# Performance work log

Hardware: AMD Instinct MI355X
Metric: run time of the kernel (lower is better)

Reference implementation:

```python
import jax, jax.numpy as jnp
import numpy as np

B, N, D, H = 8, 2048, 128, 128  # batch, num_nodes, input_size, hidden_size


def setup_inputs() -> dict:
    key = jax.random.key(0)
    ks = jax.random.split(key, 10)
    s = 1.0 / np.sqrt(H)
    u = lambda k, shape: jax.random.uniform(k, shape, jnp.float32, -s, s)
    return {
        "x": jax.random.normal(ks[0], (B, N, D), jnp.float32),
        "adj_matrix": jax.random.randint(ks[1], (B, N, N), 0, 2, jnp.int32),
        # PyTorch LSTM params, gate order (i, f, g, o); forward + backward dirs
        "w_ih_f": u(ks[2], (4 * H, D)),
        "w_hh_f": u(ks[3], (4 * H, H)),
        "b_ih_f": u(ks[4], (4 * H,)),
        "b_hh_f": u(ks[5], (4 * H,)),
        "w_ih_b": u(ks[6], (4 * H, D)),
        "w_hh_b": u(ks[7], (4 * H, H)),
        "b_ih_b": u(ks[8], (4 * H,)),
        "b_hh_b": u(ks[9], (4 * H,)),
    }


def _lstm_last_h(xp, w_hh):
    # xp: [T, B, 4H] precomputed input projection + biases; returns final h [B, H]
    b = xp.shape[1]
    h0 = jnp.zeros((b, H), xp.dtype)
    c0 = jnp.zeros((b, H), xp.dtype)

    def step(carry, xt):
        h, c = carry
        gates = xt + h @ w_hh.T
        i, f, g, o = jnp.split(gates, 4, axis=-1)
        c = jax.nn.sigmoid(f) * c + jax.nn.sigmoid(i) * jnp.tanh(g)
        h = jax.nn.sigmoid(o) * jnp.tanh(c)
        return (h, c), None

    (hT, _), _ = jax.lax.scan(step, (h0, c0), xp)
    return hT


def reference(x, adj_matrix, w_ih_f, w_hh_f, b_ih_f, b_hh_f, w_ih_b, w_hh_b, b_ih_b, b_hh_b):
    x = x.astype(jnp.float32)
    a = (adj_matrix > 0).astype(jnp.float32)  # [B, N, N]
    # mean over {self} + neighbors: (x_i + sum_j a_ij x_j) / (1 + deg_i)
    deg = a.sum(-1, keepdims=True)
    xa = (x + jnp.einsum('bij,bjd->bid', a, x)) / (1.0 + deg)  # [B, N, D]

    seq = jnp.swapaxes(xa, 0, 1)  # [N, B, D], time-major over nodes
    hT_f = _lstm_last_h(seq @ w_ih_f.T + (b_ih_f + b_hh_f), w_hh_f)
    hT_b = _lstm_last_h(seq[::-1] @ w_ih_b.T + (b_ih_b + b_hh_b), w_hh_b)
    return jnp.concatenate([hT_f, hT_b], axis=-1)  # [B, 2H]
```

## Files before the change

### kernel.cpp

```cpp
#include <hip/hip_runtime.h>
#include <math.h>

#define BB 8
#define NN 2048
#define DD 128
#define HH 128

typedef float f4 __attribute__((ext_vector_type(4)));

__device__ __forceinline__ float fast_rcp(float x) { return __builtin_amdgcn_rcpf(x); }

#define TI 32
#define TJ 64

__global__ __launch_bounds__(256) void k_agg(const float* __restrict__ x,
                                             const int* __restrict__ adj,
                                             float* __restrict__ xa) {
    __shared__ __align__(16) float xs[TJ][132];
    __shared__ __align__(16) float as[TI][68];
    const int b = blockIdx.y;
    const int i0 = blockIdx.x * TI;
    const int tid = threadIdx.x;
    const int ig = tid >> 5;
    const int dg = tid & 31;
    const float* xb = x + (size_t)b * NN * DD;
    const int* ab = adj + (size_t)b * NN * NN;

    float acc[4][4];
    float deg[4];
#pragma unroll
    for (int i = 0; i < 4; ++i) {
        deg[i] = 0.f;
#pragma unroll
        for (int d = 0; d < 4; ++d) acc[i][d] = 0.f;
    }

    for (int j0 = 0; j0 < NN; j0 += TJ) {
#pragma unroll
        for (int k = 0; k < 8; ++k) {
            int idx = tid + k * 256;
            int row = idx >> 5, c4 = idx & 31;
            float4 v = *(const float4*)(xb + (size_t)(j0 + row) * DD + c4 * 4);
            *(float4*)(&xs[row][c4 * 4]) = v;
        }
#pragma unroll
        for (int k = 0; k < 2; ++k) {
            int idx = tid + k * 256;
            int row = idx >> 4, c4 = idx & 15;
            int4 v = *(const int4*)(ab + (size_t)(i0 + row) * NN + j0 + c4 * 4);
            float4 f;
            f.x = v.x > 0 ? 1.f : 0.f;
            f.y = v.y > 0 ? 1.f : 0.f;
            f.z = v.z > 0 ? 1.f : 0.f;
            f.w = v.w > 0 ? 1.f : 0.f;
            *(float4*)(&as[row][c4 * 4]) = f;
        }
        __syncthreads();
#pragma unroll 4
        for (int jq = 0; jq < TJ; jq += 4) {
            float4 av[4], xv[4];
#pragma unroll
            for (int i = 0; i < 4; ++i) av[i] = *(const float4*)(&as[ig * 4 + i][jq]);
#pragma unroll
            for (int jj = 0; jj < 4; ++jj) xv[jj] = *(const float4*)(&xs[jq + jj][dg * 4]);
#pragma unroll
            for (int i = 0; i < 4; ++i) {
                const float* ap = (const float*)&av[i];
#pragma unroll
                for (int jj = 0; jj < 4; ++jj) {
                    float a = ap[jj];
                    const float* xp4 = (const float*)&xv[jj];
                    deg[i] += a;
                    acc[i][0] = fmaf(a, xp4[0], acc[i][0]);
                    acc[i][1] = fmaf(a, xp4[1], acc[i][1]);
                    acc[i][2] = fmaf(a, xp4[2], acc[i][2]);
                    acc[i][3] = fmaf(a, xp4[3], acc[i][3]);
                }
            }
        }
        __syncthreads();
    }
#pragma unroll
    for (int i = 0; i < 4; ++i) {
        int gi = i0 + ig * 4 + i;
        float r = fast_rcp(1.f + deg[i]);
        float4 xv = *(const float4*)(xb + (size_t)gi * DD + dg * 4);
        float4 o;
        o.x = (xv.x + acc[i][0]) * r;
        o.y = (xv.y + acc[i][1]) * r;
        o.z = (xv.z + acc[i][2]) * r;
        o.w = (xv.w + acc[i][3]) * r;
        *(float4*)(xa + ((size_t)b * NN + gi) * DD + dg * 4) = o;
    }
}

#define MT 64
#define GT 32

__global__ __launch_bounds__(256) void k_proj(const float* __restrict__ xa,
                                              const float* __restrict__ wif,
                                              const float* __restrict__ wib,
                                              const float* __restrict__ bif,
                                              const float* __restrict__ bhf,
                                              const float* __restrict__ bib,
                                              const float* __restrict__ bhb,
                                              float* __restrict__ xpf,
                                              float* __restrict__ xpb) {
    __shared__ __align__(16) float xs[MT][132];
    __shared__ __align__(16) float wl[GT][132];
    const int r0 = blockIdx.x * MT;
    const int g0 = blockIdx.y * GT;
    const int tid = threadIdx.x;
#pragma unroll
    for (int k = 0; k < 8; ++k) {
        int idx = tid + k * 256;
        int row = idx >> 5, c4 = idx & 31;
        int r = r0 + row;
        int t = r >> 3, bb = r & 7;
        float4 v = *(const float4*)(xa + ((size_t)bb * NN + t) * DD + c4 * 4);
        *(float4*)(&xs[row][c4 * 4]) = v;
    }
#pragma unroll
    for (int k = 0; k < 4; ++k) {
        int idx = tid + k * 256;
        int row = idx >> 5, c4 = idx & 31;
        int g = g0 + row;
        const float* wsrc = (g < 512) ? (wif + (size_t)g * DD) : (wib + (size_t)(g - 512) * DD);
        *(float4*)(&wl[row][c4 * 4]) = *(const float4*)(wsrc + c4 * 4);
    }
    __syncthreads();
    const int mg = tid >> 4;
    const int gg = tid & 15;
    float acc[4][2];
#pragma unroll
    for (int i = 0; i < 4; ++i) { acc[i][0] = 0.f; acc[i][1] = 0.f; }
#pragma unroll 8
    for (int d4 = 0; d4 < 32; ++d4) {
        float4 xv[4], wv[2];
#pragma unroll
        for (int i = 0; i < 4; ++i) xv[i] = *(const float4*)(&xs[mg * 4 + i][d4 * 4]);
        wv[0] = *(const float4*)(&wl[gg * 2 + 0][d4 * 4]);
        wv[1] = *(const float4*)(&wl[gg * 2 + 1][d4 * 4]);
#pragma unroll
        for (int i = 0; i < 4; ++i) {
#pragma unroll
            for (int j = 0; j < 2; ++j) {
                acc[i][j] = fmaf(xv[i].x, wv[j].x, acc[i][j]);
                acc[i][j] = fmaf(xv[i].y, wv[j].y, acc[i][j]);
                acc[i][j] = fmaf(xv[i].z, wv[j].z, acc[i][j]);
                acc[i][j] = fmaf(xv[i].w, wv[j].w, acc[i][j]);
            }
        }
    }
#pragma unroll
    for (int j = 0; j < 2; ++j) {
        int g = g0 + gg * 2 + j;
        float bias = (g < 512) ? (bif[g] + bhf[g]) : (bib[g - 512] + bhb[g - 512]);
#pragma unroll
        for (int i = 0; i < 4; ++i) {
            int r = r0 + mg * 4 + i;
            int t = r >> 3, bb = r & 7;
            float v = acc[i][j] + bias;
            if (g < 512) {
                int p = 4 * (g & 127) + (g >> 7);
                xpf[((size_t)t * BB + bb) * 512 + p] = v;
            } else {
                int gb = g - 512;
                int p = 4 * (gb & 127) + (gb >> 7);
                xpb[((size_t)(NN - 1 - t) * BB + bb) * 512 + p] = v;
            }
        }
    }
}


#define STRG(x) #x
#define WLD(R0, R3, WOFF, IMM)                                            \
    "global_load_dwordx4 v[" STRG(R0) ":" STRG(R3) "], %[" STRG(WOFF) "], %[whs] offset:" STRG(IMM) "\n\t"
#define PKQ(H0, H1, A0, A1, B0, B1, C0, C1, D0, D1)                                        \
    "v_pk_fma_f32 v[24:25], v[" STRG(A0) ":" STRG(A1) "], v[" STRG(H0) ":" STRG(H1) "], v[24:25]\n\t" \
    "v_pk_fma_f32 v[26:27], v[" STRG(B0) ":" STRG(B1) "], v[" STRG(H0) ":" STRG(H1) "], v[26:27]\n\t" \
    "v_pk_fma_f32 v[28:29], v[" STRG(C0) ":" STRG(C1) "], v[" STRG(H0) ":" STRG(H1) "], v[28:29]\n\t" \
    "v_pk_fma_f32 v[30:31], v[" STRG(D0) ":" STRG(D1) "], v[" STRG(H0) ":" STRG(H1) "], v[30:31]\n\t"
#define PKQ0(H0, H1, A0, A1, B0, B1, C0, C1, D0, D1)                                       \
    "v_pk_mul_f32 v[24:25], v[" STRG(A0) ":" STRG(A1) "], v[" STRG(H0) ":" STRG(H1) "]\n\t" \
    "v_pk_mul_f32 v[26:27], v[" STRG(B0) ":" STRG(B1) "], v[" STRG(H0) ":" STRG(H1) "]\n\t" \
    "v_pk_mul_f32 v[28:29], v[" STRG(C0) ":" STRG(C1) "], v[" STRG(H0) ":" STRG(H1) "]\n\t" \
    "v_pk_mul_f32 v[30:31], v[" STRG(D0) ":" STRG(D1) "], v[" STRG(H0) ":" STRG(H1) "]\n\t"

__global__ __launch_bounds__(512) void k_lstm(const float* __restrict__ xpf,
                                              const float* __restrict__ xpb,
                                              const float* __restrict__ whf,
                                              const float* __restrict__ whb,
                                              float* __restrict__ out) {
    const int b = blockIdx.x;
    const int dir = blockIdx.y;
    const float* __restrict__ xp = dir ? xpb : xpf;
    const float* __restrict__ wh = dir ? whb : whf;
    const int t = threadIdx.x;
    const int q = t >> 2;
    const int jq = t & 3;

    __shared__ __align__(64) float h_lds[1088];
    for (int i = t; i < 1088; i += 512) h_lds[i] = 0.f;
    __syncthreads();

    unsigned hbase = (unsigned)(uintptr_t)&h_lds[0];
    unsigned rd0 = hbase + 672u * (unsigned)jq;
    unsigned rdd = rd0 ^ (rd0 + 2176u);
    unsigned wr0 = hbase + 2176u + 544u * (unsigned)jq + ((unsigned)q << 2);
    unsigned wrd = wr0 ^ (wr0 - 2176u);
    unsigned w0 = ((0u * 128u + (unsigned)q) * 128u + (unsigned)jq * 32u) * 4u;
    unsigned w1 = ((1u * 128u + (unsigned)q) * 128u + (unsigned)jq * 32u) * 4u;
    unsigned w2 = ((2u * 128u + (unsigned)q) * 128u + (unsigned)jq * 32u) * 4u;
    unsigned w3 = ((3u * 128u + (unsigned)q) * 128u + (unsigned)jq * 32u) * 4u;
    unsigned xoff = (unsigned)(b * 512 + t) * 4u + 16384u;
    float xp0v = xp[(size_t)b * 512 + t];
    float s0 = (jq == 0) ? 1.f : 0.f;
    float s1 = (jq == 1) ? 1.f : 0.f;
    float s2 = (jq == 2) ? 1.f : 0.f;
    float s3 = (jq == 3) ? 1.f : 0.f;
    float mlv = (jq == 2) ? -2.8853900817779268f : -1.4426950408889634f;
    float Aav = (jq == 2) ? 2.f : 1.f;
    float Bav = (jq == 2) ? -1.f : 0.f;
    float h_out;

    asm volatile(
        "v_mov_b32 v16, 0\n\t"
        "s_movk_i32 s20, 0x800\n\t"
        "v_mov_b32 v19, %[x0]\n\t"
        "v_mov_b32 v21, %[xo]\n\t"
        "v_mov_b32 v22, %[rdb]\n\t"
        "v_mov_b32 v23, %[wrb]\n\t"
        WLD(64, 67, w0, 0) WLD(68, 71, w0, 16) WLD(72, 75, w0, 32) WLD(76, 79, w0, 48)
        WLD(80, 83, w0, 64) WLD(84, 87, w0, 80) WLD(88, 91, w0, 96) WLD(92, 95, w0, 112)
        WLD(96, 99, w1, 0) WLD(100, 103, w1, 16) WLD(104, 107, w1, 32) WLD(108, 111, w1, 48)
        WLD(112, 115, w1, 64) WLD(116, 119, w1, 80) WLD(120, 123, w1, 96) WLD(124, 127, w1, 112)
        WLD(128, 131, w2, 0) WLD(132, 135, w2, 16) WLD(136, 139, w2, 32) WLD(140, 143, w2, 48)
        WLD(144, 147, w2, 64) WLD(148, 151, w2, 80) WLD(152, 155, w2, 96) WLD(156, 159, w2, 112)
        WLD(160, 163, w3, 0) WLD(164, 167, w3, 16) WLD(168, 171, w3, 32) WLD(172, 175, w3, 48)
        WLD(176, 179, w3, 64) WLD(180, 183, w3, 80) WLD(184, 187, w3, 96) WLD(188, 191, w3, 112)
        "s_waitcnt vmcnt(0)\n\t"
        "LSTM_TOP%=:\n\t"
        "global_load_dword v20, v21, %[xps]\n\t"
        "ds_read_b128 v[32:35], v22\n\t"
        "ds_read_b128 v[36:39], v22 offset:16\n\t"
        "ds_read_b128 v[40:43], v22 offset:32\n\t"
        "ds_read_b128 v[44:47], v22 offset:48\n\t"
        "ds_read_b128 v[48:51], v22 offset:64\n\t"
        "ds_read_b128 v[52:55], v22 offset:80\n\t"
        "ds_read_b128 v[56:59], v22 offset:96\n\t"
        "ds_read_b128 v[60:63], v22 offset:112\n\t"
        "v_xor_b32 v22, %[rdd], v22\n\t"
        "v_add_u32 v21, 0x4000, v21\n\t"
        "s_waitcnt lgkmcnt(7)\n\t"
        PKQ0(32, 33, 64, 65, 96, 97, 128, 129, 160, 161)
        PKQ(34, 35, 66, 67, 98, 99, 130, 131, 162, 163)
        "s_waitcnt lgkmcnt(6)\n\t"
        PKQ(36, 37, 68, 69, 100, 101, 132, 133, 164, 165)
        PKQ(38, 39, 70, 71, 102, 103, 134, 135, 166, 167)
        "s_waitcnt lgkmcnt(5)\n\t"
        PKQ(40, 41, 72, 73, 104, 105, 136, 137, 168, 169)
        PKQ(42, 43, 74, 75, 106, 107, 138, 139, 170, 171)
        "s_waitcnt lgkmcnt(4)\n\t"
        PKQ(44, 45, 76, 77, 108, 109, 140, 141, 172, 173)
        PKQ(46, 47, 78, 79, 110, 111, 142, 143, 174, 175)
        "s_waitcnt lgkmcnt(3)\n\t"
        PKQ(48, 49, 80, 81, 112, 113, 144, 145, 176, 177)
        PKQ(50, 51, 82, 83, 114, 115, 146, 147, 178, 179)
        "s_waitcnt lgkmcnt(2)\n\t"
        PKQ(52, 53, 84, 85, 116, 117, 148, 149, 180, 181)
        PKQ(54, 55, 86, 87, 118, 119, 150, 151, 182, 183)
        "s_waitcnt lgkmcnt(1)\n\t"
        PKQ(56, 57, 88, 89, 120, 121, 152, 153, 184, 185)
        PKQ(58, 59, 90, 91, 122, 123, 154, 155, 186, 187)
        "s_waitcnt lgkmcnt(0)\n\t"
        PKQ(60, 61, 92, 93, 124, 125, 156, 157, 188, 189)
        PKQ(62, 63, 94, 95, 126, 127, 158, 159, 190, 191)
        "v_add_f32 v8, v24, v25\n\t"
        "v_add_f32 v9, v26, v27\n\t"
        "v_add_f32 v10, v28, v29\n\t"
        "v_add_f32 v11, v30, v31\n\t"
        "v_mov_b32_dpp v12, v8 quad_perm:[1,0,3,2] row_mask:0xf bank_mask:0xf\n\t"
        "v_mov_b32_dpp v13, v9 quad_perm:[1,0,3,2] row_mask:0xf bank_mask:0xf\n\t"
        "v_mov_b32_dpp v14, v10 quad_perm:[1,0,3,2] row_mask:0xf bank_mask:0xf\n\t"
        "v_mov_b32_dpp v15, v11 quad_perm:[1,0,3,2] row_mask:0xf bank_mask:0xf\n\t"
        "v_add_f32 v8, v8, v12\n\t"
        "v_add_f32 v9, v9, v13\n\t"
        "v_add_f32 v10, v10, v14\n\t"
        "v_add_f32 v11, v11, v15\n\t"
        "v_mov_b32_dpp v12, v8 quad_perm:[2,3,0,1] row_mask:0xf bank_mask:0xf\n\t"
        "v_mov_b32_dpp v13, v9 quad_perm:[2,3,0,1] row_mask:0xf bank_mask:0xf\n\t"
        "v_mov_b32_dpp v14, v10 quad_perm:[2,3,0,1] row_mask:0xf bank_mask:0xf\n\t"
        "v_mov_b32_dpp v15, v11 quad_perm:[2,3,0,1] row_mask:0xf bank_mask:0xf\n\t"
        "v_add_f32 v8, v8, v12\n\t"
        "v_add_f32 v9, v9, v13\n\t"
        "v_add_f32 v10, v10, v14\n\t"
        "v_add_f32 v11, v11, v15\n\t"
        "v_mul_f32 v12, %[s0], v8\n\t"
        "v_fma_f32 v12, %[s1], v9, v12\n\t"
        "v_fma_f32 v12, %[s2], v10, v12\n\t"
        "v_fma_f32 v12, %[s3], v11, v12\n\t"
        "v_add_f32 v12, v12, v19\n\t"
        "v_mul_f32 v13, %[ml], v12\n\t"
        "v_exp_f32 v13, v13\n\t"
        "s_nop 1\n\t"
        "v_add_f32 v13, 1.0, v13\n\t"
        "v_rcp_f32 v13, v13\n\t"
        "s_nop 1\n\t"
        "v_fma_f32 v12, %[Aa], v13, %[Ba]\n\t"
        "s_nop 1\n\t"
        "v_mov_b32_dpp v13, v12 quad_perm:[0,0,0,0] row_mask:0xf bank_mask:0xf\n\t"
        "v_mov_b32_dpp v14, v12 quad_perm:[2,2,2,2] row_mask:0xf bank_mask:0xf\n\t"
        "v_mov_b32_dpp v15, v12 quad_perm:[1,1,1,1] row_mask:0xf bank_mask:0xf\n\t"
        "v_mov_b32_dpp v17, v12 quad_perm:[3,3,3,3] row_mask:0xf bank_mask:0xf\n\t"
        "v_mul_f32 v13, v13, v14\n\t"
        "v_fma_f32 v16, v15, v16, v13\n\t"
        "v_mul_f32 v14, 0xc038aa3b, v16\n\t"
        "v_exp_f32 v14, v14\n\t"
        "s_nop 1\n\t"
        "v_add_f32 v14, 1.0, v14\n\t"
        "v_rcp_f32 v14, v14\n\t"
        "s_nop 1\n\t"
        "v_fma_f32 v14, 2.0, v14, -1.0\n\t"
        "v_mul_f32 v17, v14, v17\n\t"
        "ds_write_b32 v23, v17\n\t"
        "s_waitcnt vmcnt(0) lgkmcnt(0)\n\t"
        "v_mov_b32 v19, v20\n\t"
        "s_barrier\n\t"
        "v_xor_b32 v23, %[wrd], v23\n\t"
        "s_sub_u32 s20, s20, 1\n\t"
        "s_cmp_lg_u32 s20, 0\n\t"
        "s_cbranch_scc1 LSTM_TOP%=\n\t"
        "v_mov_b32 %[ho], v17\n\t"
        : [ho] "=v"(h_out)
        : [w0] "v"(w0), [w1] "v"(w1), [w2] "v"(w2), [w3] "v"(w3),
          [whs] "s"(wh), [xps] "s"(xp),
          [xo] "v"(xoff), [rdb] "v"(rd0), [wrb] "v"(wr0),
          [rdd] "v"(rdd), [wrd] "v"(wrd), [x0] "v"(xp0v),
          [s0] "v"(s0), [s1] "v"(s1), [s2] "v"(s2), [s3] "v"(s3),
          [ml] "v"(mlv), [Aa] "v"(Aav), [Ba] "v"(Bav)
        : "memory", "vcc", "scc", "s20",
          "v8", "v9", "v10", "v11", "v12", "v13", "v14", "v15", "v16", "v17",
          "v18", "v19", "v20", "v21", "v22", "v23", "v24", "v25", "v26", "v27",
          "v28", "v29", "v30", "v31", "v32", "v33", "v34", "v35", "v36", "v37",
          "v38", "v39", "v40", "v41", "v42", "v43", "v44", "v45", "v46", "v47",
          "v48", "v49", "v50", "v51", "v52", "v53", "v54", "v55", "v56", "v57",
          "v58", "v59", "v60", "v61", "v62", "v63", "v64", "v65", "v66", "v67",
          "v68", "v69", "v70", "v71", "v72", "v73", "v74", "v75", "v76", "v77",
          "v78", "v79", "v80", "v81", "v82", "v83", "v84", "v85", "v86", "v87",
          "v88", "v89", "v90", "v91", "v92", "v93", "v94", "v95", "v96", "v97",
          "v98", "v99", "v100", "v101", "v102", "v103", "v104", "v105", "v106", "v107",
          "v108", "v109", "v110", "v111", "v112", "v113", "v114", "v115", "v116", "v117",
          "v118", "v119", "v120", "v121", "v122", "v123", "v124", "v125", "v126", "v127",
          "v128", "v129", "v130", "v131", "v132", "v133", "v134", "v135", "v136", "v137",
          "v138", "v139", "v140", "v141", "v142", "v143", "v144", "v145", "v146", "v147",
          "v148", "v149", "v150", "v151", "v152", "v153", "v154", "v155", "v156", "v157",
          "v158", "v159", "v160", "v161", "v162", "v163", "v164", "v165", "v166", "v167",
          "v168", "v169", "v170", "v171", "v172", "v173", "v174", "v175", "v176", "v177",
          "v178", "v179", "v180", "v181", "v182", "v183", "v184", "v185", "v186", "v187",
          "v188", "v189", "v190", "v191");

    if (jq == 0) out[(size_t)b * 256 + dir * HH + q] = h_out;
}

extern "C" void kernel_launch(void* const* d_in, const int* in_sizes, int n_in,
                              void* d_out, int out_size, void* d_ws, size_t ws_size,
                              hipStream_t stream) {
    const float* x = (const float*)d_in[0];
    const int* adj = (const int*)d_in[1];
    const float* wif = (const float*)d_in[2];
    const float* whf = (const float*)d_in[3];
    const float* bif = (const float*)d_in[4];
    const float* bhf = (const float*)d_in[5];
    const float* wib = (const float*)d_in[6];
    const float* whb = (const float*)d_in[7];
    const float* bib = (const float*)d_in[8];
    const float* bhb = (const float*)d_in[9];
    float* out = (float*)d_out;

    float* xpf = (float*)d_ws;
    float* xpb = xpf + (size_t)NN * BB * 512;
    float* xa = xpb + (size_t)NN * BB * 512;

    k_agg<<<dim3(NN / TI, BB), 256, 0, stream>>>(x, adj, xa);
    k_proj<<<dim3((NN * BB) / MT, 1024 / GT), 256, 0, stream>>>(xa, wif, wib, bif, bhf, bib, bhb,
                                                                xpf, xpb);
    k_lstm<<<dim3(BB, 2), 512, 0, stream>>>(xpf, xpb, whf, whb, out);
}
```

Before: 1.363 ms.

## Move neighbor aggregation to bf16 split MFMA with transposed x and identity-folded adjacency

Replaces the FP32 FMA aggregation kernel with an MFMA-based one. A new pre-pass transposes x and splits it into bf16 high and low parts, stored in the workspace that is later reused for the projection output. The adjacency plus identity is encoded as bf16 0/1/2 and multiplied on matrix cores, with degree computed by an MFMA against ones. The LSTM loop's barrier is also moved ahead of the global-load wait so outstanding loads can overlap the barrier. Precision drops somewhat, since x is held as a two-term bf16 split while the adjacency weights stay exact.

```diff
diff --git a/kernel.cpp b/kernel.cpp
--- a/kernel.cpp
+++ b/kernel.cpp
@@ -7,91 +7,144 @@
 #define HH 128
 
 typedef float f4 __attribute__((ext_vector_type(4)));
+typedef __attribute__((ext_vector_type(8))) short s16x8;
+typedef __attribute__((ext_vector_type(8))) unsigned short u16x8;
 
 __device__ __forceinline__ float fast_rcp(float x) { return __builtin_amdgcn_rcpf(x); }
 
-#define TI 32
-#define TJ 64
-
-__global__ __launch_bounds__(256) void k_agg(const float* __restrict__ x,
-                                             const int* __restrict__ adj,
-                                             float* __restrict__ xa) {
-    __shared__ __align__(16) float xs[TJ][132];
-    __shared__ __align__(16) float as[TI][68];
+__device__ __forceinline__ void bsplit(float x, unsigned short& h, unsigned short& l) {
+    unsigned u = __float_as_uint(x);
+    unsigned r = u + 0x7FFFu + ((u >> 16) & 1u);
+    h = (unsigned short)(r >> 16);
+    float xh = __uint_as_float(((unsigned)h) << 16);
+    float d = x - xh;
+    unsigned u2 = __float_as_uint(d);
+    unsigned r2 = u2 + 0x7FFFu + ((u2 >> 16) & 1u);
+    l = (unsigned short)(r2 >> 16);
+}
+
+__global__ __launch_bounds__(256) void k_xT(const float* __restrict__ x,
+                                            unsigned short* __restrict__ xth,
+                                            unsigned short* __restrict__ xtl) {
+    __shared__ __align__(16) unsigned short th[32][72];
+    __shared__ __align__(16) unsigned short tl[32][72];
+    const int n0 = blockIdx.x * 64;
+    const int d0 = blockIdx.y * 32;
+    const int b = blockIdx.z;
+    const int tid = threadIdx.x;
+    {
+        const int nl = tid & 63, dseg = tid >> 6;
+        const float* xp = x + ((size_t)b * NN + n0 + nl) * DD + d0 + dseg * 8;
+        float4 v0 = *(const float4*)(xp);
+        float4 v1 = *(const float4*)(xp + 4);
+        const float* vv = (const float*)&v0;
+#pragma unroll
+        for (int j = 0; j < 4; ++j) {
+            unsigned short hh, ll;
+            bsplit(vv[j], hh, ll);
+            th[dseg * 8 + j][nl] = hh;
+            tl[dseg * 8 + j][nl] = ll;
+        }
+        const float* vw = (const float*)&v1;
+#pragma unroll
+        for (int j = 0; j < 4; ++j) {
+            unsigned short hh, ll;
+            bsplit(vw[j], hh, ll);
+            th[dseg * 8 + 4 + j][nl] = hh;
+            tl[dseg * 8 + 4 + j][nl] = ll;
+        }
+    }
+    __syncthreads();
+    {
+        const int dl = tid >> 3, nseg = tid & 7;
+        u16x8 vh = *(const u16x8*)&th[dl][nseg * 8];
+        u16x8 vl = *(const u16x8*)&tl[dl][nseg * 8];
+        size_t off = ((size_t)b * DD + d0 + dl) * NN + n0 + nseg * 8;
+        *(u16x8*)(xth + off) = vh;
+        *(u16x8*)(xtl + off) = vl;
+    }
+}
+
+__global__ __launch_bounds__(256) void k_agg2(const int* __restrict__ adj,
+                                              const unsigned short* __restrict__ xth,
+                                              const unsigned short* __restrict__ xtl,
+                                              float* __restrict__ xa) {
+    __shared__ __align__(16) unsigned short Al[64][40];
+    __shared__ __align__(16) unsigned short Xh[128][40];
+    __shared__ __align__(16) unsigned short Xl[128][40];
     const int b = blockIdx.y;
-    const int i0 = blockIdx.x * TI;
+    const int i0 = blockIdx.x * 64;
     const int tid = threadIdx.x;
-    const int ig = tid >> 5;
-    const int dg = tid & 31;
-    const float* xb = x + (size_t)b * NN * DD;
-    const int* ab = adj + (size_t)b * NN * NN;
-
-    float acc[4][4];
-    float deg[4];
-#pragma unroll
-    for (int i = 0; i < 4; ++i) {
-        deg[i] = 0.f;
-#pragma unroll
-        for (int d = 0; d < 4; ++d) acc[i][d] = 0.f;
-    }
-
-    for (int j0 = 0; j0 < NN; j0 += TJ) {
-#pragma unroll
-        for (int k = 0; k < 8; ++k) {
-            int idx = tid + k * 256;
-            int row = idx >> 5, c4 = idx & 31;
-            float4 v = *(const float4*)(xb + (size_t)(j0 + row) * DD + c4 * 4);
-            *(float4*)(&xs[row][c4 * 4]) = v;
-        }
-#pragma unroll
-        for (int k = 0; k < 2; ++k) {
-            int idx = tid + k * 256;
-            int row = idx >> 4, c4 = idx & 15;
-            int4 v = *(const int4*)(ab + (size_t)(i0 + row) * NN + j0 + c4 * 4);
-            float4 f;
-            f.x = v.x > 0 ? 1.f : 0.f;
-            f.y = v.y > 0 ? 1.f : 0.f;
-            f.z = v.z > 0 ? 1.f : 0.f;
-            f.w = v.w > 0 ? 1.f : 0.f;
-            *(float4*)(&as[row][c4 * 4]) = f;
+    const int wave = tid >> 6, lane = tid & 63;
+    const int ar = tid >> 2, aks = (tid & 3) * 8;
+    const int xd = tid >> 1, xks = (tid & 1) * 16;
+    const int* ap = adj + ((size_t)b * NN + i0 + ar) * NN + aks;
+    const unsigned short* hp = xth + ((size_t)b * DD + xd) * NN + xks;
+    const unsigned short* lp = xtl + ((size_t)b * DD + xd) * NN + xks;
+
+    f4 acc[8], dacc;
+#pragma unroll
+    for (int t = 0; t < 8; ++t) acc[t] = {0.f, 0.f, 0.f, 0.f};
+    dacc = {0.f, 0.f, 0.f, 0.f};
+    const short onebf = (short)0x3F80;
+    s16x8 ones = {onebf, onebf, onebf, onebf, onebf, onebf, onebf, onebf};
+
+    int4 a0 = *(const int4*)(ap);
+    int4 a1 = *(const int4*)(ap + 4);
+    u16x8 h0 = *(const u16x8*)(hp);
+    u16x8 h1 = *(const u16x8*)(hp + 8);
+    u16x8 l0 = *(const u16x8*)(lp);
+    u16x8 l1 = *(const u16x8*)(lp + 8);
+
+    for (int k0 = 0; k0 < NN; k0 += 32) {
+        {
+            u16x8 w;
+            const int* av0 = (const int*)&a0;
+            const int* av1 = (const int*)&a1;
+            int colb = k0 + aks, myrow = i0 + ar;
+#pragma unroll
+            for (int j = 0; j < 4; ++j) {
+                int c0 = (av0[j] > 0 ? 1 : 0) + (myrow == colb + j ? 1 : 0);
+                int c1 = (av1[j] > 0 ? 1 : 0) + (myrow == colb + 4 + j ? 1 : 0);
+                w[j] = c0 == 0 ? 0 : (c0 == 1 ? 0x3F80 : 0x4000);
+                w[4 + j] = c1 == 0 ? 0 : (c1 == 1 ? 0x3F80 : 0x4000);
+            }
+            *(u16x8*)&Al[ar][aks] = w;
+            *(u16x8*)&Xh[xd][xks] = h0;
+            *(u16x8*)&Xh[xd][xks + 8] = h1;
+            *(u16x8*)&Xl[xd][xks] = l0;
+            *(u16x8*)&Xl[xd][xks + 8] = l1;
         }
         __syncthreads();
-#pragma unroll 4
-        for (int jq = 0; jq < TJ; jq += 4) {
-            float4 av[4], xv[4];
-#pragma unroll
-            for (int i = 0; i < 4; ++i) av[i] = *(const float4*)(&as[ig * 4 + i][jq]);
-#pragma unroll
-            for (int jj = 0; jj < 4; ++jj) xv[jj] = *(const float4*)(&xs[jq + jj][dg * 4]);
-#pragma unroll
-            for (int i = 0; i < 4; ++i) {
-                const float* ap = (const float*)&av[i];
-#pragma unroll
-                for (int jj = 0; jj < 4; ++jj) {
-                    float a = ap[jj];
-                    const float* xp4 = (const float*)&xv[jj];
-                    deg[i] += a;
-                    acc[i][0] = fmaf(a, xp4[0], acc[i][0]);
-                    acc[i][1] = fmaf(a, xp4[1], acc[i][1]);
-                    acc[i][2] = fmaf(a, xp4[2], acc[i][2]);
-                    acc[i][3] = fmaf(a, xp4[3], acc[i][3]);
-                }
-            }
-        }
+        if (k0 + 32 < NN) {
+            a0 = *(const int4*)(ap + k0 + 32);
+            a1 = *(const int4*)(ap + k0 + 36);
+            h0 = *(const u16x8*)(hp + k0 + 32);
+            h1 = *(const u16x8*)(hp + k0 + 40);
+            l0 = *(const u16x8*)(lp + k0 + 32);
+            l1 = *(const u16x8*)(lp + k0 + 40);
+        }
+        s16x8 afr = *(const s16x8*)&Al[16 * wave + (lane & 15)][(lane >> 4) * 8];
+#pragma unroll
+        for (int t = 0; t < 8; ++t) {
+            s16x8 bh = *(const s16x8*)&Xh[16 * t + (lane & 15)][(lane >> 4) * 8];
+            s16x8 bl = *(const s16x8*)&Xl[16 * t + (lane & 15)][(lane >> 4) * 8];
+            acc[t] = __builtin_amdgcn_mfma_f32_16x16x32_bf16(afr, bh, acc[t], 0, 0, 0);
+            acc[t] = __builtin_amdgcn_mfma_f32_16x16x32_bf16(afr, bl, acc[t], 0, 0, 0);
+        }
+        dacc = __builtin_amdgcn_mfma_f32_16x16x32_bf16(afr, ones, dacc, 0, 0, 0);
         __syncthreads();
     }
-#pragma unroll
-    for (int i = 0; i < 4; ++i) {
-        int gi = i0 + ig * 4 + i;
-        float r = fast_rcp(1.f + deg[i]);
-        float4 xv = *(const float4*)(xb + (size_t)gi * DD + dg * 4);
-        float4 o;
-        o.x = (xv.x + acc[i][0]) * r;
-        o.y = (xv.y + acc[i][1]) * r;
-        o.z = (xv.z + acc[i][2]) * r;
-        o.w = (xv.w + acc[i][3]) * r;
-        *(float4*)(xa + ((size_t)b * NN + gi) * DD + dg * 4) = o;
-    }
+    float inv[4];
+#pragma unroll
+    for (int r = 0; r < 4; ++r) inv[r] = fast_rcp(dacc[r]);
+#pragma unroll
+    for (int t = 0; t < 8; ++t)
+#pragma unroll
+        for (int r = 0; r < 4; ++r) {
+            int row = i0 + 16 * wave + (lane >> 4) * 4 + r;
+            xa[((size_t)b * NN + row) * DD + 16 * t + (lane & 15)] = acc[t][r] * inv[r];
+        }
 }
 
 #define MT 64
@@ -325,9 +378,10 @@
         "v_fma_f32 v14, 2.0, v14, -1.0\n\t"
         "v_mul_f32 v17, v14, v17\n\t"
         "ds_write_b32 v23, v17\n\t"
-        "s_waitcnt vmcnt(0) lgkmcnt(0)\n\t"
+        "s_waitcnt lgkmcnt(0)\n\t"
+        "s_barrier\n\t"
+        "s_waitcnt vmcnt(0)\n\t"
         "v_mov_b32 v19, v20\n\t"
-        "s_barrier\n\t"
         "v_xor_b32 v23, %[wrd], v23\n\t"
         "s_sub_u32 s20, s20, 1\n\t"
         "s_cmp_lg_u32 s20, 0\n\t"
@@ -382,8 +436,11 @@
     float* xpf = (float*)d_ws;
     float* xpb = xpf + (size_t)NN * BB * 512;
     float* xa = xpb + (size_t)NN * BB * 512;
-
-    k_agg<<<dim3(NN / TI, BB), 256, 0, stream>>>(x, adj, xa);
+    unsigned short* xth = (unsigned short*)xpf;
+    unsigned short* xtl = xth + (size_t)BB * DD * NN;
+
+    k_xT<<<dim3(NN / 64, DD / 32, BB), 256, 0, stream>>>(x, xth, xtl);
+    k_agg2<<<dim3(NN / 64, BB), 256, 0, stream>>>(adj, xth, xtl, xa);
     k_proj<<<dim3((NN * BB) / MT, 1024 / GT), 256, 0, stream>>>(xa, wif, wib, bif, bhf, bib, bhb,
                                                                 xpf, xpb);
     k_lstm<<<dim3(BB, 2), 512, 0, stream>>>(xpf, xpb, whf, whb, out);
```

Measured after the change: 1.247 ms. -8.5%, faster.
